# Kernel optimization log

Measured on AMD Instinct MI355X. Metric: run time of the kernel, lower is better.

The kernel has to match this reference:

```python
import jax, jax.numpy as jnp
import numpy as np

S, B, FEAT, HAND, H, C = 16, 128, 2048, 63, 1024, 1000


def _lstm_step(h, c, xt, wih, whh, bih, bhh):
    # xt: [B, in], h/c: [B, H]; PyTorch gate order i, f, g, o
    gates = xt @ wih.T + bih + h @ whh.T + bhh
    i, f, g, o = jnp.split(gates, 4, axis=-1)
    c_new = jax.nn.sigmoid(f) * c + jax.nn.sigmoid(i) * jnp.tanh(g)
    h_new = jax.nn.sigmoid(o) * jnp.tanh(c_new)
    return h_new, c_new


def setup_inputs() -> dict:
    key = jax.random.key(0)
    ks = jax.random.split(key, 16)
    def u(k, shape, fan_in):
        s = 1.0 / np.sqrt(fan_in)
        return jax.random.uniform(k, shape, jnp.float32, -s, s)
    return {
        "feats": jax.random.normal(ks[0], (S, B, FEAT), jnp.float32),
        "lh": jax.random.normal(ks[1], (S, B, HAND), jnp.float32),
        "rh": jax.random.normal(ks[2], (S, B, HAND), jnp.float32),
        "act": jax.random.randint(ks[3], (B,), 0, C),
        "fc1_w": u(ks[4], (H, FEAT), FEAT), "fc1_b": u(ks[5], (H,), FEAT),
        "fch_w": u(ks[6], (H, 2 * HAND), 2 * HAND), "fch_b": u(ks[7], (H,), 2 * HAND),
        "roll_wih": u(ks[8], (4 * H, 2 * H), H), "roll_whh": u(ks[9], (4 * H, H), H),
        "roll_bih": u(ks[10], (4 * H,), H), "roll_bhh": u(ks[11], (4 * H,), H),
        "unroll_wih": u(ks[12], (4 * H, 2 * H), H), "unroll_whh": u(ks[13], (4 * H, H), H),
        "unroll_bih": u(ks[14], (4 * H,), H), "unroll_bhh": u(ks[15], (4 * H,), H),
        "cls_w": u(jax.random.fold_in(key, 100), (C, H), H),
        "cls_b": u(jax.random.fold_in(key, 101), (C,), H),
    }


def reference(feats, lh, rh, act, fc1_w, fc1_b, fch_w, fch_b,
              roll_wih, roll_whh, roll_bih, roll_bhh,
              unroll_wih, unroll_whh, unroll_bih, unroll_bhh,
              cls_w, cls_b):
    # dropout layers are identities in eval mode
    hands = jnp.concatenate([lh, rh], axis=-1)          # [S,B,126]
    hproj = hands @ fch_w.T + fch_b                      # [S,B,H]
    xproj = feats @ fc1_w.T + fc1_b                      # [S,B,H]
    x = jnp.concatenate([xproj, hproj], axis=-1)         # [S,B,2H]

    h0 = jnp.zeros((B, H), x.dtype)
    c0 = jnp.zeros((B, H), x.dtype)

    # rolling LSTM: collect hidden & cell at every timestep
    def roll_step(carry, xt):
        h, c = carry
        h, c = _lstm_step(h, c, xt, roll_wih, roll_whh, roll_bih, roll_bhh)
        return (h, c), (h, c)
    _, (hs, cs) = jax.lax.scan(roll_step, (h0, c0), x)   # each [S,B,H]

    # unrolling LSTM: from state (hs[t], cs[t]), feed x[t] repeated (S-t+1) times
    def unroll_one(xt, h_init, c_init):
        def step(carry, _):
            h, c = carry
            h, c = _lstm_step(h, c, xt, unroll_wih, unroll_whh, unroll_bih, unroll_bhh)
            return (h, c), h
        _, hseq = jax.lax.scan(step, (h_init, c_init), None, length=S + 1)
        return hseq                                       # [S+1,B,H]
    hs_all = jax.vmap(unroll_one)(x, hs, cs)              # [S,S+1,B,H]
    # last hidden of a length-(S-t+1) rollout is index S-t
    h_n = hs_all[jnp.arange(S), S - jnp.arange(S)]        # [S,B,H]

    xp = jnp.transpose(h_n, (1, 0, 2))                    # [B,S,H]
    y = xp @ cls_w.T + cls_b                              # [B,S,C]
    out = y[:, -1, :]                                     # [B,C]
    pred = jnp.argmax(out, axis=1)
    logz = jax.nn.logsumexp(out, axis=-1)
    loss = jnp.mean(logz - jnp.take_along_axis(out, act[:, None], axis=1)[:, 0])
    return out, pred, loss
```

## Files before the change

### kernel.cpp

```cpp
#include <hip/hip_runtime.h>
#include <math.h>


typedef __attribute__((ext_vector_type(8))) _Float16 f16x8;
typedef __attribute__((ext_vector_type(4))) _Float16 f16x4;
typedef __attribute__((ext_vector_type(4))) float     f32x4;

typedef __attribute__((address_space(1))) const void as1c_void;
typedef __attribute__((address_space(3))) void       as3_void;
#define GLOAD_LDS16(g, l) \
    __builtin_amdgcn_global_load_lds((as1c_void*)(g), (as3_void*)(l), 16, 0, 0)

#define NBLK 256

template<int BN, int OUTMODE, bool BIAS>
__global__ __launch_bounds__(256)
void gemm_mfma(const _Float16* __restrict__ A, int lda, int aLoOff,
               const _Float16* __restrict__ W, int ldw, int wLoOff,
               const float* __restrict__ bias,
               void* __restrict__ Cout, int ldc, int Nout,
               int ksize, long cOffPerZ)
{
    constexpr int BM = 128, BK = 64;
    constexpr int WTN = BN / 2;
    constexpr int NF  = WTN / 16;

    __shared__ _Float16 As[BM * BK];
    __shared__ _Float16 Ws[BN * BK];

    const int tid  = threadIdx.x;
    const int wave = tid >> 6, lane = tid & 63;
    const int wr = wave >> 1, wc = wave & 1;
    const int bn = blockIdx.x * BN;
    const int bm = blockIdx.y * BM;
    const long kbase = (long)blockIdx.z * ksize;

    f32x4 acc[4][NF];
    #pragma unroll
    for (int i = 0; i < 4; ++i)
        #pragma unroll
        for (int j = 0; j < NF; ++j) acc[i][j] = (f32x4){0.f, 0.f, 0.f, 0.f};

    const int srow  = tid >> 3;
    const int sbyte = (tid & 7) * 16;
    const int swzS  = (srow & 7) << 4;

    const int arow0 = wr * 64 + (lane & 15);
    const int abyte = (lane >> 4) * 16;

    for (int seg = 0; seg < 3; ++seg) {
        const int aOff = (seg == 1) ? aLoOff : 0;
        const int wOff = (seg == 2) ? wLoOff : 0;

        for (int k0 = 0; k0 < ksize; k0 += BK) {
            const long kg = kbase + k0;
            #pragma unroll
            for (int r = 0; r < 4; ++r) {
                const _Float16* src = A + ((long)(bm + 32*r + srow) * lda
                                           + aOff + kg) + ((sbyte ^ swzS) >> 1);
                GLOAD_LDS16(src, (char*)As + r*4096 + wave*1024);
            }
            #pragma unroll
            for (int r = 0; r < BN/32; ++r) {
                const _Float16* src = W + ((long)(bn + 32*r + srow) * ldw
                                           + wOff + kg) + ((sbyte ^ swzS) >> 1);
                GLOAD_LDS16(src, (char*)Ws + r*4096 + wave*1024);
            }
            __syncthreads();
            #pragma unroll
            for (int kk = 0; kk < 2; ++kk) {
                f16x8 af[4], bfr[NF];
                #pragma unroll
                for (int mi = 0; mi < 4; ++mi) {
                    const int row = arow0 + mi*16;
                    const int byi = (kk*64 + abyte) ^ ((row & 7) << 4);
                    af[mi] = *(const f16x8*)((const char*)As + row*128 + byi);
                }
                #pragma unroll
                for (int ni = 0; ni < NF; ++ni) {
                    const int row = wc*WTN + ni*16 + (lane & 15);
                    const int byi = (kk*64 + abyte) ^ ((row & 7) << 4);
                    bfr[ni] = *(const f16x8*)((const char*)Ws + row*128 + byi);
                }
                #pragma unroll
                for (int mi = 0; mi < 4; ++mi)
                    #pragma unroll
                    for (int ni = 0; ni < NF; ++ni)
                        acc[mi][ni] = __builtin_amdgcn_mfma_f32_16x16x32_f16(
                            af[mi], bfr[ni], acc[mi][ni], 0, 0, 0);
            }
            __syncthreads();
        }
    }

    float*     Cf = (float*)Cout + blockIdx.z * cOffPerZ;
    _Float16*  Ch = (_Float16*)Cout;
    #pragma unroll
    for (int mi = 0; mi < 4; ++mi) {
        #pragma unroll
        for (int ni = 0; ni < NF; ++ni) {
            const int col = bn + wc*WTN + ni*16 + (lane & 15);
            if (col < Nout) {
                const float bv = BIAS ? bias[col] : 0.f;
                #pragma unroll
                for (int r = 0; r < 4; ++r) {
                    const int row = bm + wr*64 + mi*16 + (lane >> 4)*4 + r;
                    const float v = acc[mi][ni][r] + bv;
                    if constexpr (OUTMODE == 1) {
                        _Float16 hi = (_Float16)v;
                        Ch[(long)row * ldc + col]         = hi;
                        Ch[(long)row * ldc + ldc/2 + col] = (_Float16)(v - (float)hi);
                    } else if constexpr (OUTMODE == 2) {
                        const int t = row >> 7, b = row & 127;
                        const int q = col >> 10, j = col & 1023;
                        Cf[(long)t*524288 + (long)(j>>2)*2048
                           + b*16 + (j&3)*4 + q] = v;
                    } else {
                        Cf[(long)row * ldc + col] = v;
                    }
                }
            }
        }
    }
}

__global__ __launch_bounds__(512)
void lstm_persistent(const _Float16* __restrict__ whh,
                     const _Float16* __restrict__ uwhh,
                     const float* __restrict__ xgT,
                     const float* __restrict__ ugT,
                     _Float16* __restrict__ hbufs,
                     _Float16* __restrict__ hfin,
                     unsigned* __restrict__ bar)
{
    constexpr int WROW = 4112;
    __shared__ alignas(16) char Wl[16 * WROW];
    __shared__ float Gl[2048];

    const int tid  = threadIdx.x;
    const int wave = tid >> 6, lane = tid & 63;
    const int bid  = (int)blockIdx.x;
    const int j0   = bid * 4;

    auto stageW = [&](const _Float16* __restrict__ src) {
        const int seg = wave & 3;
        #pragma unroll
        for (int it = 0; it < 8; ++it) {
            const int g = it * 2 + (wave >> 2);
            const long G = (long)(g >> 2) * 1024 + j0 + (g & 3);
            const _Float16* s = src + G * 2048 + seg * 512 + lane * 8;
            GLOAD_LDS16(s, Wl + g * WROW + seg * 1024);
        }
    };

    auto poll = [&](unsigned ph) {
        if (wave == 0) {
            const unsigned long long* f64 = (const unsigned long long*)bar;
            for (;;) {
                unsigned long long a = __hip_atomic_load(f64 + lane,
                    __ATOMIC_RELAXED, __HIP_MEMORY_SCOPE_AGENT);
                unsigned long long b = __hip_atomic_load(f64 + 64 + lane,
                    __ATOMIC_RELAXED, __HIP_MEMORY_SCOPE_AGENT);
                const int ok = ((unsigned)a >= ph) && ((unsigned)(a >> 32) >= ph)
                            && ((unsigned)b >= ph) && ((unsigned)(b >> 32) >= ph);
                if (__all(ok)) break;
                __builtin_amdgcn_s_sleep(1);
            }
        }
        __syncthreads();
    };

    const int b_c = tid >> 2;
    const int jj  = tid & 3;
    float c_reg = 0.f;

    auto do_cell = [&](float4 xgv, bool addGl, _Float16* hout, bool fin) {
        float g4[4] = {xgv.x, xgv.y, xgv.z, xgv.w};
        if (addGl) {
            #pragma unroll
            for (int q = 0; q < 4; ++q) g4[q] += Gl[b_c * 16 + q * 4 + jj];
        }
        const float si = 1.f / (1.f + __expf(-g4[0]));
        const float sf = 1.f / (1.f + __expf(-g4[1]));
        const float so = 1.f / (1.f + __expf(-g4[3]));
        float e = __expf(-2.f * fabsf(g4[2]));
        float tg = (1.f - e) / (1.f + e); tg = g4[2] < 0.f ? -tg : tg;
        c_reg = sf * c_reg + si * tg;
        e = __expf(-2.f * fabsf(c_reg));
        float tc = (1.f - e) / (1.f + e); tc = c_reg < 0.f ? -tc : tc;
        const float hv = so * tc;
        union { _Float16 f; unsigned short u; } cv; cv.f = (_Float16)hv;
        if (fin) {
            hout[(long)b_c * 2048 + j0 + jj]        = cv.f;
            hout[(long)b_c * 2048 + 1024 + j0 + jj] = (_Float16)(hv - (float)cv.f);
        } else {
            int w  = cv.u;
            int p2 = w | (__shfl_xor(w, 1) << 16);
            int q2 = __shfl_xor(p2, 2);
            if (jj == 0) {
                unsigned long long v = (unsigned)p2
                                     | ((unsigned long long)(unsigned)q2 << 32);
                __hip_atomic_store((unsigned long long*)(hout + (long)b_c*1024 + j0),
                                   v, __ATOMIC_RELAXED, __HIP_MEMORY_SCOPE_AGENT);
            }
        }
    };

    stageW(whh);

    const long xoff = (long)bid * 2048 + b_c * 16 + jj * 4;
    { float4 x0 = *(const float4*)(xgT + xoff); do_cell(x0, false, hbufs, false); }
    asm volatile("s_waitcnt vmcnt(0)" ::: "memory");
    __syncthreads();
    if (tid == 0)
        __hip_atomic_store(bar + bid, 1u, __ATOMIC_RELAXED,
                           __HIP_MEMORY_SCOPE_AGENT);

    const int arow = wave * 16 + (lane & 15);
    const int koff = (lane >> 4) * 8;
    const char* wrow = Wl + (lane & 15) * WROW + (lane >> 4) * 16;

    for (int p = 1; p < 18; ++p) {
        if (p == 16) {
            stageW(uwhh);
            asm volatile("s_waitcnt vmcnt(0)" ::: "memory");
        }
        poll((unsigned)p);

        const float* xsrc = (p <= 15) ? xgT + (long)p * 524288 : ugT;
        const float4 xcur = *(const float4*)(xsrc + xoff);

        const _Float16* hp = hbufs + (long)(p - 1) * 131072
                           + (long)arow * 1024 + koff;
        f16x8 af[32];
        #pragma unroll
        for (int i = 0; i < 32; ++i)
            af[i] = *(const f16x8*)(hp + (long)i * 32);

        f32x4 acch = (f32x4){0.f,0.f,0.f,0.f};
        f32x4 accl = (f32x4){0.f,0.f,0.f,0.f};
        #pragma unroll
        for (int i = 0; i < 32; ++i) {
            const f16x8 bhi = *(const f16x8*)(wrow + i * 64);
            const f16x8 blo = *(const f16x8*)(wrow + 2048 + i * 64);
            acch = __builtin_amdgcn_mfma_f32_16x16x32_f16(af[i], bhi, acch, 0, 0, 0);
            accl = __builtin_amdgcn_mfma_f32_16x16x32_f16(af[i], blo, accl, 0, 0, 0);
        }
        #pragma unroll
        for (int r = 0; r < 4; ++r)
            Gl[(wave * 16 + (lane >> 4) * 4 + r) * 16 + (lane & 15)]
                = acch[r] + accl[r];
        __syncthreads();

        do_cell(xcur, true, (p == 17) ? hfin : hbufs + (long)p * 131072, p == 17);
        asm volatile("s_waitcnt vmcnt(0)" ::: "memory");
        __syncthreads();
        if (tid == 0)
            __hip_atomic_store(bar + bid, (unsigned)(p + 1),
                               __ATOMIC_RELAXED, __HIP_MEMORY_SCOPE_AGENT);
    }
}

__global__ __launch_bounds__(256)
void convert_split_g(const float* __restrict__ src, _Float16* __restrict__ dst,
                     int sh, long n4)
{
    const long i = (long)blockIdx.x * 256 + threadIdx.x;
    if (i >= n4) return;
    const long row = i >> sh;
    const long k4  = i & ((1L << sh) - 1);
    const float4 v = ((const float4*)src)[i];
    const float vv[4] = {v.x, v.y, v.z, v.w};
    f16x4 hi, lo;
    #pragma unroll
    for (int j = 0; j < 4; ++j) {
        hi[j] = (_Float16)vv[j];
        lo[j] = (_Float16)(vv[j] - (float)hi[j]);
    }
    ((f16x4*)dst)[(row << (sh + 1)) + k4]              = hi;
    ((f16x4*)dst)[(row << (sh + 1)) + (1L << sh) + k4] = lo;
}

__global__ __launch_bounds__(256)
void bias_sum(const float* __restrict__ a1, const float* __restrict__ b1,
              const float* __restrict__ a2, const float* __restrict__ b2,
              float* __restrict__ o1, float* __restrict__ o2)
{
    const int i = blockIdx.x * 256 + threadIdx.x;
    if (i < 4096) { o1[i] = a1[i] + b1[i]; o2[i] = a2[i] + b2[i]; }
}

__global__ __launch_bounds__(256)
void hproj_kernel(const float* __restrict__ lh, const float* __restrict__ rh,
                  const float* __restrict__ fchw, const float* __restrict__ fchb,
                  _Float16* __restrict__ x)
{
    __shared__ float hs[16][126];
    const int brow = blockIdx.x * 16;
    for (int idx = threadIdx.x; idx < 16 * 126; idx += 256) {
        const int r = idx / 126, k = idx % 126;
        const int grow = brow + r;
        hs[r][k] = (k < 63) ? lh[(long)grow * 63 + k]
                            : rh[(long)grow * 63 + (k - 63)];
    }
    __syncthreads();
    for (int j = threadIdx.x; j < 1024; j += 256) {
        float acc[16];
        #pragma unroll
        for (int r = 0; r < 16; ++r) acc[r] = 0.f;
        const float* wrow = fchw + (long)j * 126;
        for (int k = 0; k < 126; ++k) {
            const float w = wrow[k];
            #pragma unroll
            for (int r = 0; r < 16; ++r) acc[r] = fmaf(w, hs[r][k], acc[r]);
        }
        const float b = fchb[j];
        #pragma unroll
        for (int r = 0; r < 16; ++r) {
            const float v = acc[r] + b;
            const _Float16 hi = (_Float16)v;
            x[(long)(brow + r) * 4096 + 1024 + j] = hi;
            x[(long)(brow + r) * 4096 + 3072 + j] = (_Float16)(v - (float)hi);
        }
    }
}

__global__ __launch_bounds__(256)
void reduce4_bias(const float* __restrict__ part, const float* __restrict__ bias,
                  float* __restrict__ out)
{
    const int t = blockIdx.x * 256 + threadIdx.x;
    const long o = (long)t * 4;
    const int b   = (int)(o >> 12);
    const int rem = (int)(o & 4095);
    const int q   = rem >> 10, jb = rem & 1023;
    float4 s = *(const float4*)(part + o);
    #pragma unroll
    for (int p = 1; p < 4; ++p) {
        const float4 v = *(const float4*)(part + (long)p*524288 + o);
        s.x += v.x; s.y += v.y; s.z += v.z; s.w += v.w;
    }
    const float4 bb = *(const float4*)(bias + rem);
    const float sv[4] = {s.x + bb.x, s.y + bb.y, s.z + bb.z, s.w + bb.w};
    #pragma unroll
    for (int e = 0; e < 4; ++e) {
        const int j = jb + e;
        out[(long)(j >> 2) * 2048 + b * 16 + (j & 3) * 4 + q] = sv[e];
    }
}

__global__ __launch_bounds__(256)
void head_kernel(const float* __restrict__ logits, const int* __restrict__ act,
                 float* __restrict__ d_out, float* __restrict__ lossbuf)
{
    const int b = blockIdx.x;
    const int tid = threadIdx.x;
    const float* row = logits + (long)b * 1000;

    float mx = -1e30f; int mi = 1 << 30;
    for (int j = tid; j < 1000; j += 256) {
        const float v = row[j];
        if (v > mx) { mx = v; mi = j; }
    }
    __shared__ float smx[256];
    __shared__ int   smi[256];
    smx[tid] = mx; smi[tid] = mi;
    __syncthreads();
    for (int s = 128; s > 0; s >>= 1) {
        if (tid < s) {
            const float v2 = smx[tid + s]; const int i2 = smi[tid + s];
            if (v2 > smx[tid] || (v2 == smx[tid] && i2 < smi[tid])) {
                smx[tid] = v2; smi[tid] = i2;
            }
        }
        __syncthreads();
    }
    const float gmx = smx[0];
    const int   gmi = smi[0];
    __syncthreads();

    float partial = 0.f;
    for (int j = tid; j < 1000; j += 256) partial += __expf(row[j] - gmx);
    smx[tid] = partial;
    __syncthreads();
    for (int s = 128; s > 0; s >>= 1) {
        if (tid < s) smx[tid] += smx[tid + s];
        __syncthreads();
    }
    if (tid == 0) {
        d_out[128000 + b] = (float)gmi;
        lossbuf[b] = gmx + logf(smx[0]) - row[act[b]];
    }
}

__global__ __launch_bounds__(128)
void loss_reduce(const float* __restrict__ lossbuf, float* __restrict__ d_out)
{
    __shared__ float s[128];
    const int tid = threadIdx.x;
    s[tid] = lossbuf[tid];
    __syncthreads();
    for (int k = 64; k > 0; k >>= 1) {
        if (tid < k) s[tid] += s[tid + k];
        __syncthreads();
    }
    if (tid == 0) d_out[128128] = s[0] / 128.f;
}

extern "C" void kernel_launch(void* const* d_in, const int* in_sizes, int n_in,
                              void* d_out, int out_size, void* d_ws, size_t ws_size,
                              hipStream_t stream)
{
    const float* feats    = (const float*)d_in[0];
    const float* lh       = (const float*)d_in[1];
    const float* rh       = (const float*)d_in[2];
    const int*   act      = (const int*)  d_in[3];
    const float* fc1_w    = (const float*)d_in[4];
    const float* fc1_b    = (const float*)d_in[5];
    const float* fch_w    = (const float*)d_in[6];
    const float* fch_b    = (const float*)d_in[7];
    const float* roll_wih = (const float*)d_in[8];
    const float* roll_whh = (const float*)d_in[9];
    const float* roll_bih = (const float*)d_in[10];
    const float* roll_bhh = (const float*)d_in[11];
    const float* un_wih   = (const float*)d_in[12];
    const float* un_whh   = (const float*)d_in[13];
    const float* un_bih   = (const float*)d_in[14];
    const float* un_bhh   = (const float*)d_in[15];
    const float* cls_w    = (const float*)d_in[16];
    const float* cls_b    = (const float*)d_in[17];

    float* out = (float*)d_out;
    char* ws = (char*)d_ws;
    size_t o = 0;
    auto alloc = [&](size_t b) { size_t r = o; o += (b + 255) & ~(size_t)255; return r; };

    _Float16* x_h2     = (_Float16*)(ws + alloc(2048ul*4096*2));
    char*     regB     = ws + alloc(2048ul*4096*2);
    char*     regC     = ws + alloc(4096ul*4096*2);
    _Float16* whhr_h2  = (_Float16*)(ws + alloc(4096ul*2048*2));
    char*     regE     = ws + alloc(16ul*128*4096*4);
    float*    ugate    = (float*)   (ws + alloc(128ul*4096*4));
    _Float16* h_h2     = (_Float16*)(ws + alloc(128ul*2048*2));
    float*    rollb    = (float*)   (ws + alloc(4096*4));
    float*    unb      = (float*)   (ws + alloc(4096*4));
    float*    lossbuf  = (float*)   (ws + alloc(128*4));
    unsigned* barctr   = (unsigned*)(ws + alloc(2048));

    _Float16* feats_h2 = (_Float16*)regB;
    float*    part     = (float*)regB;
    _Float16* clsw_h2  = (_Float16*)(regB + (8ul<<20));
    _Float16* wihr_h2  = (_Float16*)regC;
    _Float16* unwhh_h2 = (_Float16*)regC;
    _Float16* hbufs    = (_Float16*)(regC + (16ul<<20));
    _Float16* fc1w_h2  = (_Float16*)regE;
    _Float16* unwih_h2 = (_Float16*)regE;
    float*    xgates   = (float*)regE;

    convert_split_g<<<4096, 256, 0, stream>>>(feats,    feats_h2, 9, 1048576);
    convert_split_g<<<8192, 256, 0, stream>>>(roll_wih, wihr_h2,  9, 2097152);
    convert_split_g<<<4096, 256, 0, stream>>>(roll_whh, whhr_h2,  8, 1048576);
    convert_split_g<<<2048, 256, 0, stream>>>(fc1_w,    fc1w_h2,  9, 524288);
    bias_sum<<<16, 256, 0, stream>>>(roll_bih, roll_bhh, un_bih, un_bhh, rollb, unb);
    hipMemsetAsync(barctr, 0, 2048, stream);

    gemm_mfma<128, 1, true><<<dim3(8, 16, 1), 256, 0, stream>>>(
        feats_h2, 4096, 2048, fc1w_h2, 4096, 2048, fc1_b,
        x_h2, 4096, 1024, 2048, 0);
    hproj_kernel<<<128, 256, 0, stream>>>(lh, rh, fch_w, fch_b, x_h2);

    convert_split_g<<<8192, 256, 0, stream>>>(un_wih, unwih_h2, 9, 2097152);
    gemm_mfma<64, 0, false><<<dim3(64, 1, 4), 256, 0, stream>>>(
        x_h2 + 15l*128*4096, 4096, 2048, unwih_h2, 4096, 2048, nullptr,
        part, 4096, 4096, 512, 524288);
    reduce4_bias<<<512, 256, 0, stream>>>(part, unb, ugate);

    gemm_mfma<128, 2, true><<<dim3(32, 16, 1), 256, 0, stream>>>(
        x_h2, 4096, 2048, wihr_h2, 4096, 2048, rollb, xgates, 4096, 4096, 2048, 0);

    convert_split_g<<<4096, 256, 0, stream>>>(un_whh, unwhh_h2, 8, 1048576);
    convert_split_g<<<1000, 256, 0, stream>>>(cls_w,  clsw_h2,  8, 256000);

    lstm_persistent<<<NBLK, 512, 0, stream>>>(whhr_h2, unwhh_h2,
                                              xgates, ugate, hbufs, h_h2, barctr);

    gemm_mfma<64, 0, true><<<dim3(16, 1, 1), 256, 0, stream>>>(
        h_h2, 2048, 1024, clsw_h2, 2048, 1024, cls_b, out, 1000, 1000, 1024, 0);
    head_kernel<<<128, 256, 0, stream>>>(out, act, out, lossbuf);
    loss_reduce<<<1, 128, 0, stream>>>(lossbuf, out);
}
```

Before: 624.4 us.

## Fuse input-gate GEMMs into persistent LSTM kernel, overlapped after barrier release

Removes the standalone roll/unroll input-projection GEMMs, the fp32-to-split-fp16 conversions of the input weights, and the partial-sum reduce kernel. Each persistent LSTM block now computes its own 4-gate slice of x@Wih for the next timestep right after publishing its barrier flag, so that work can hide behind the wait for other blocks. Weights are read directly in fp32 and split on the fly into hi/lo fp16 parts. The cost is that every block re-reads the fp32 weight rows each step and does conversion ALU work inside the recurrent loop. If that work does not fit in the barrier wait, it lengthens the critical path.

```diff
diff --git a/kernel.cpp b/kernel.cpp
--- a/kernel.cpp
+++ b/kernel.cpp
@@ -110,11 +110,6 @@
                         _Float16 hi = (_Float16)v;
                         Ch[(long)row * ldc + col]         = hi;
                         Ch[(long)row * ldc + ldc/2 + col] = (_Float16)(v - (float)hi);
-                    } else if constexpr (OUTMODE == 2) {
-                        const int t = row >> 7, b = row & 127;
-                        const int q = col >> 10, j = col & 1023;
-                        Cf[(long)t*524288 + (long)(j>>2)*2048
-                           + b*16 + (j&3)*4 + q] = v;
                     } else {
                         Cf[(long)row * ldc + col] = v;
                     }
@@ -127,8 +122,11 @@
 __global__ __launch_bounds__(512)
 void lstm_persistent(const _Float16* __restrict__ whh,
                      const _Float16* __restrict__ uwhh,
-                     const float* __restrict__ xgT,
-                     const float* __restrict__ ugT,
+                     const _Float16* __restrict__ x_h2,
+                     const float* __restrict__ wih,
+                     const float* __restrict__ uwih,
+                     const float* __restrict__ rollb,
+                     const float* __restrict__ unb,
                      _Float16* __restrict__ hbufs,
                      _Float16* __restrict__ hfin,
                      unsigned* __restrict__ bar)
@@ -136,6 +134,7 @@
     constexpr int WROW = 4112;
     __shared__ alignas(16) char Wl[16 * WROW];
     __shared__ float Gl[2048];
+    __shared__ float xgL[2][2048];
 
     const int tid  = threadIdx.x;
     const int wave = tid >> 6, lane = tid & 63;
@@ -170,15 +169,52 @@
         __syncthreads();
     };
 
+    const int arow = wave * 16 + (lane & 15);
+    const int koff = (lane >> 4) * 8;
+    const int s_   = lane & 15;
+    const int G_   = (s_ >> 2) * 1024 + j0 + (s_ & 3);
+    const float biasR = rollb[G_];
+    const float biasU = unb[G_];
+
     const int b_c = tid >> 2;
     const int jj  = tid & 3;
     float c_reg = 0.f;
 
-    auto do_cell = [&](float4 xgv, bool addGl, _Float16* hout, bool fin) {
-        float g4[4] = {xgv.x, xgv.y, xgv.z, xgv.w};
-        if (addGl) {
+    auto xg_gemm = [&](int t, const float* __restrict__ Wsrc, float bias,
+                       float* __restrict__ dst) {
+        const _Float16* xr = x_h2 + ((long)(t * 128 + arow)) * 4096 + koff;
+        const float*    Wp = Wsrc + (long)G_ * 2048 + koff;
+        f32x4 acc = (f32x4){bias, bias, bias, bias};
+        #pragma unroll 4
+        for (int i = 0; i < 64; ++i) {
+            const f16x8 ahi = *(const f16x8*)(xr + i * 32);
+            const f16x8 alo = *(const f16x8*)(xr + 2048 + i * 32);
+            const float4 w0 = *(const float4*)(Wp + i * 32);
+            const float4 w1 = *(const float4*)(Wp + i * 32 + 4);
+            const float ww[8] = {w0.x, w0.y, w0.z, w0.w, w1.x, w1.y, w1.z, w1.w};
+            f16x8 whi, wlo;
             #pragma unroll
-            for (int q = 0; q < 4; ++q) g4[q] += Gl[b_c * 16 + q * 4 + jj];
+            for (int e = 0; e < 8; ++e) {
+                const _Float16 h = (_Float16)ww[e];
+                whi[e] = h;
+                wlo[e] = (_Float16)(ww[e] - (float)h);
+            }
+            acc = __builtin_amdgcn_mfma_f32_16x16x32_f16(ahi, whi, acc, 0, 0, 0);
+            acc = __builtin_amdgcn_mfma_f32_16x16x32_f16(alo, whi, acc, 0, 0, 0);
+            acc = __builtin_amdgcn_mfma_f32_16x16x32_f16(ahi, wlo, acc, 0, 0, 0);
+        }
+        #pragma unroll
+        for (int r = 0; r < 4; ++r)
+            dst[(wave * 16 + (lane >> 4) * 4 + r) * 16 + s_] = acc[r];
+    };
+
+    auto do_cell = [&](const float* __restrict__ xgbuf, bool addGl,
+                       _Float16* hout, bool fin) {
+        float g4[4];
+        #pragma unroll
+        for (int q = 0; q < 4; ++q) {
+            g4[q] = xgbuf[b_c * 16 + q * 4 + jj];
+            if (addGl) g4[q] += Gl[b_c * 16 + q * 4 + jj];
         }
         const float si = 1.f / (1.f + __expf(-g4[0]));
         const float sf = 1.f / (1.f + __expf(-g4[1]));
@@ -207,17 +243,18 @@
     };
 
     stageW(whh);
-
-    const long xoff = (long)bid * 2048 + b_c * 16 + jj * 4;
-    { float4 x0 = *(const float4*)(xgT + xoff); do_cell(x0, false, hbufs, false); }
+    xg_gemm(0, wih, biasR, xgL[0]);
+    asm volatile("s_waitcnt vmcnt(0)" ::: "memory");
+    __syncthreads();
+
+    do_cell(xgL[0], false, hbufs, false);
     asm volatile("s_waitcnt vmcnt(0)" ::: "memory");
     __syncthreads();
     if (tid == 0)
         __hip_atomic_store(bar + bid, 1u, __ATOMIC_RELAXED,
                            __HIP_MEMORY_SCOPE_AGENT);
-
-    const int arow = wave * 16 + (lane & 15);
-    const int koff = (lane >> 4) * 8;
+    xg_gemm(1, wih, biasR, xgL[1]);
+
     const char* wrow = Wl + (lane & 15) * WROW + (lane >> 4) * 16;
 
     for (int p = 1; p < 18; ++p) {
@@ -226,9 +263,6 @@
             asm volatile("s_waitcnt vmcnt(0)" ::: "memory");
         }
         poll((unsigned)p);
-
-        const float* xsrc = (p <= 15) ? xgT + (long)p * 524288 : ugT;
-        const float4 xcur = *(const float4*)(xsrc + xoff);
 
         const _Float16* hp = hbufs + (long)(p - 1) * 131072
                            + (long)arow * 1024 + koff;
@@ -252,12 +286,17 @@
                 = acch[r] + accl[r];
         __syncthreads();
 
-        do_cell(xcur, true, (p == 17) ? hfin : hbufs + (long)p * 131072, p == 17);
-        asm volatile("s_waitcnt vmcnt(0)" ::: "memory");
-        __syncthreads();
-        if (tid == 0)
-            __hip_atomic_store(bar + bid, (unsigned)(p + 1),
-                               __ATOMIC_RELAXED, __HIP_MEMORY_SCOPE_AGENT);
+        const float* xgb = (p >= 16) ? xgL[0] : xgL[p & 1];
+        do_cell(xgb, true, (p == 17) ? hfin : hbufs + (long)p * 131072, p == 17);
+        if (p < 17) {
+            asm volatile("s_waitcnt vmcnt(0)" ::: "memory");
+            __syncthreads();
+            if (tid == 0)
+                __hip_atomic_store(bar + bid, (unsigned)(p + 1),
+                                   __ATOMIC_RELAXED, __HIP_MEMORY_SCOPE_AGENT);
+            if (p < 15)       xg_gemm(p + 1, wih,  biasR, xgL[(p + 1) & 1]);
+            else if (p == 15) xg_gemm(15,    uwih, biasU, xgL[0]);
+        }
     }
 }
 
@@ -322,30 +361,6 @@
             x[(long)(brow + r) * 4096 + 1024 + j] = hi;
             x[(long)(brow + r) * 4096 + 3072 + j] = (_Float16)(v - (float)hi);
         }
-    }
-}
-
-__global__ __launch_bounds__(256)
-void reduce4_bias(const float* __restrict__ part, const float* __restrict__ bias,
-                  float* __restrict__ out)
-{
-    const int t = blockIdx.x * 256 + threadIdx.x;
-    const long o = (long)t * 4;
-    const int b   = (int)(o >> 12);
-    const int rem = (int)(o & 4095);
-    const int q   = rem >> 10, jb = rem & 1023;
-    float4 s = *(const float4*)(part + o);
-    #pragma unroll
-    for (int p = 1; p < 4; ++p) {
-        const float4 v = *(const float4*)(part + (long)p*524288 + o);
-        s.x += v.x; s.y += v.y; s.z += v.z; s.w += v.w;
-    }
-    const float4 bb = *(const float4*)(bias + rem);
-    const float sv[4] = {s.x + bb.x, s.y + bb.y, s.z + bb.z, s.w + bb.w};
-    #pragma unroll
-    for (int e = 0; e < 4; ++e) {
-        const int j = jb + e;
-        out[(long)(j >> 2) * 2048 + b * 16 + (j & 3) * 4 + q] = sv[e];
     }
 }
 
@@ -436,31 +451,23 @@
     auto alloc = [&](size_t b) { size_t r = o; o += (b + 255) & ~(size_t)255; return r; };
 
     _Float16* x_h2     = (_Float16*)(ws + alloc(2048ul*4096*2));
-    char*     regB     = ws + alloc(2048ul*4096*2);
-    char*     regC     = ws + alloc(4096ul*4096*2);
+    _Float16* feats_h2 = (_Float16*)(ws + alloc(2048ul*4096*2));
     _Float16* whhr_h2  = (_Float16*)(ws + alloc(4096ul*2048*2));
-    char*     regE     = ws + alloc(16ul*128*4096*4);
-    float*    ugate    = (float*)   (ws + alloc(128ul*4096*4));
+    _Float16* unwhh_h2 = (_Float16*)(ws + alloc(4096ul*2048*2));
+    _Float16* fc1w_h2  = (_Float16*)(ws + alloc(1024ul*4096*2));
+    _Float16* clsw_h2  = (_Float16*)(ws + alloc(1000ul*2048*2));
+    _Float16* hbufs    = (_Float16*)(ws + alloc(17ul*131072*2));
     _Float16* h_h2     = (_Float16*)(ws + alloc(128ul*2048*2));
     float*    rollb    = (float*)   (ws + alloc(4096*4));
     float*    unb      = (float*)   (ws + alloc(4096*4));
     float*    lossbuf  = (float*)   (ws + alloc(128*4));
     unsigned* barctr   = (unsigned*)(ws + alloc(2048));
 
-    _Float16* feats_h2 = (_Float16*)regB;
-    float*    part     = (float*)regB;
-    _Float16* clsw_h2  = (_Float16*)(regB + (8ul<<20));
-    _Float16* wihr_h2  = (_Float16*)regC;
-    _Float16* unwhh_h2 = (_Float16*)regC;
-    _Float16* hbufs    = (_Float16*)(regC + (16ul<<20));
-    _Float16* fc1w_h2  = (_Float16*)regE;
-    _Float16* unwih_h2 = (_Float16*)regE;
-    float*    xgates   = (float*)regE;
-
     convert_split_g<<<4096, 256, 0, stream>>>(feats,    feats_h2, 9, 1048576);
-    convert_split_g<<<8192, 256, 0, stream>>>(roll_wih, wihr_h2,  9, 2097152);
     convert_split_g<<<4096, 256, 0, stream>>>(roll_whh, whhr_h2,  8, 1048576);
+    convert_split_g<<<4096, 256, 0, stream>>>(un_whh,   unwhh_h2, 8, 1048576);
     convert_split_g<<<2048, 256, 0, stream>>>(fc1_w,    fc1w_h2,  9, 524288);
+    convert_split_g<<<1000, 256, 0, stream>>>(cls_w,    clsw_h2,  8, 256000);
     bias_sum<<<16, 256, 0, stream>>>(roll_bih, roll_bhh, un_bih, un_bhh, rollb, unb);
     hipMemsetAsync(barctr, 0, 2048, stream);
 
@@ -469,20 +476,9 @@
         x_h2, 4096, 1024, 2048, 0);
     hproj_kernel<<<128, 256, 0, stream>>>(lh, rh, fch_w, fch_b, x_h2);
 
-    convert_split_g<<<8192, 256, 0, stream>>>(un_wih, unwih_h2, 9, 2097152);
-    gemm_mfma<64, 0, false><<<dim3(64, 1, 4), 256, 0, stream>>>(
-        x_h2 + 15l*128*4096, 4096, 2048, unwih_h2, 4096, 2048, nullptr,
-        part, 4096, 4096, 512, 524288);
-    reduce4_bias<<<512, 256, 0, stream>>>(part, unb, ugate);
-
-    gemm_mfma<128, 2, true><<<dim3(32, 16, 1), 256, 0, stream>>>(
-        x_h2, 4096, 2048, wihr_h2, 4096, 2048, rollb, xgates, 4096, 4096, 2048, 0);
-
-    convert_split_g<<<4096, 256, 0, stream>>>(un_whh, unwhh_h2, 8, 1048576);
-    convert_split_g<<<1000, 256, 0, stream>>>(cls_w,  clsw_h2,  8, 256000);
-
-    lstm_persistent<<<NBLK, 512, 0, stream>>>(whhr_h2, unwhh_h2,
-                                              xgates, ugate, hbufs, h_h2, barctr);
+    lstm_persistent<<<NBLK, 512, 0, stream>>>(
+        whhr_h2, unwhh_h2, x_h2, roll_wih, un_wih, rollb, unb,
+        hbufs, h_h2, barctr);
 
     gemm_mfma<64, 0, true><<<dim3(16, 1, 1), 256, 0, stream>>>(
         h_h2, 2048, 1024, clsw_h2, 2048, 1024, cls_b, out, 1000, 1000, 1024, 0);
```

After: 1.352 ms. 116% more time.
